# Performance work log

Measured on AMD Instinct MI355X. Metric: run time of the kernel, lower is better.

The kernel has to match this reference:

```python
import jax, jax.numpy as jnp
import numpy as np

B, S, H = 2, 2048, 2048
NH, NKV, HD = 32, 8, 64          # num_heads, num_kv_heads, head_dim
G = NH // NKV                     # GQA group size
NEG = -1e9


def setup_inputs() -> dict:
    key = jax.random.key(0)
    ks = jax.random.split(key, 8)
    x = jax.random.normal(ks[0], (B, S, H), dtype=jnp.float32)
    # real RoPE frequencies: theta = 10000 ** (-2i/hd)
    inv_freq = 1.0 / (10000.0 ** (np.arange(0, HD, 2, dtype=np.float32) / HD))
    angles = np.arange(S, dtype=np.float32)[:, None] * inv_freq[None, :]  # [S, HD//2]
    freqs_cos = jnp.asarray(np.cos(angles))
    freqs_sin = jnp.asarray(np.sin(angles))
    # additive causal mask [S, S]
    mask = jnp.where(jnp.tril(jnp.ones((S, S), dtype=bool)), 0.0, NEG).astype(jnp.float32)
    sc = 0.02
    Wq = jax.random.normal(ks[1], (NH * HD, H), dtype=jnp.float32) * sc
    bq = jax.random.normal(ks[2], (NH * HD,), dtype=jnp.float32) * sc
    Wk = jax.random.normal(ks[3], (NKV * HD, H), dtype=jnp.float32) * sc
    bk = jax.random.normal(ks[4], (NKV * HD,), dtype=jnp.float32) * sc
    Wv = jax.random.normal(ks[5], (NKV * HD, H), dtype=jnp.float32) * sc
    bv = jax.random.normal(ks[6], (NKV * HD,), dtype=jnp.float32) * sc
    Wo = jax.random.normal(ks[7], (H, NH * HD), dtype=jnp.float32) * sc
    return {"x": x, "freqs_cos": freqs_cos, "freqs_sin": freqs_sin, "mask": mask,
            "Wq": Wq, "bq": bq, "Wk": Wk, "bk": bk, "Wv": Wv, "bv": bv, "Wo": Wo}


def _rotate_half(t):
    h = t.shape[-1] // 2
    return jnp.concatenate([-t[..., h:], t[..., :h]], axis=-1)


def reference(x, freqs_cos, freqs_sin, mask, Wq, bq, Wk, bk, Wv, bv, Wo):
    b, s, _ = x.shape
    q = (x @ Wq.T + bq).reshape(b, s, NH, HD)
    k = (x @ Wk.T + bk).reshape(b, s, NKV, HD)
    v = (x @ Wv.T + bv).reshape(b, s, NKV, HD)
    # RoPE (rotate_half style): cos/sin duplicated along last dim -> [1, s, 1, HD]
    cos = jnp.concatenate([freqs_cos, freqs_cos], axis=-1)[None, :, None, :]
    sin = jnp.concatenate([freqs_sin, freqs_sin], axis=-1)[None, :, None, :]
    q = q * cos + _rotate_half(q) * sin
    k = k * cos + _rotate_half(k) * sin
    # GQA: view q as [b, s, NKV, G, HD]; avoids repeat_interleave of K/V (same math)
    q5 = q.reshape(b, s, NKV, G, HD)
    scores = jnp.einsum('bqhgd,bkhd->bhgqk', q5, k) / jnp.sqrt(jnp.float32(HD))
    scores = scores + mask  # broadcast [s, s] over [b, h, g, s, s]
    p = jax.nn.softmax(scores.astype(jnp.float32), axis=-1).astype(q.dtype)
    out = jnp.einsum('bhgqk,bkhd->bqhgd', p, v).reshape(b, s, NH * HD)
    return out @ Wo.T
```

## Files before the change

### kernel.cpp

```cpp
#include <hip/hip_runtime.h>
#include <hip/hip_bf16.h>
#include <cstddef>
#include <cstdint>

#define B_   2
#define S_   2048
#define H_   2048
#define NH_  32
#define NKV_ 8
#define HD_  64

typedef __attribute__((ext_vector_type(8))) short short8;
typedef __attribute__((ext_vector_type(4))) float v4f;
typedef __attribute__((ext_vector_type(16))) float v16f;

#define MAXC 48.0f
#define QSCALE 0.18033688011112042f

__device__ __forceinline__ unsigned short f2b(float f) {
    unsigned int u = __float_as_uint(f);
    u += 0x7FFFu + ((u >> 16) & 1u);
    return (unsigned short)(u >> 16);
}
__device__ __forceinline__ unsigned int pkbf(float a, float b) {
    __hip_bfloat162 h = __float22bfloat162_rn(float2{a, b});
    return *(unsigned int*)&h;
}
__device__ __forceinline__ float fexp2(float x) {
#if __has_builtin(__builtin_amdgcn_exp2f)
    return __builtin_amdgcn_exp2f(x);
#else
    return exp2f(x);
#endif
}
__device__ __forceinline__ v4f mfma16(short8 a, short8 b, v4f c) {
    return __builtin_amdgcn_mfma_f32_16x16x32_bf16(a, b, c, 0, 0, 0);
}
__device__ __forceinline__ v16f mfma32(short8 a, short8 b, v16f c) {
    return __builtin_amdgcn_mfma_f32_32x32x16_bf16(a, b, c, 0, 0, 0);
}
__device__ __forceinline__ void gll16(void* lds, const void* g) {
    __builtin_amdgcn_global_load_lds(
        (const __attribute__((address_space(1))) unsigned int*)g,
        (__attribute__((address_space(3))) unsigned int*)lds, 16, 0, 0);
}

__global__ __launch_bounds__(256) void convert_all(
    const float* __restrict__ x, const float* __restrict__ wq,
    const float* __restrict__ wk, const float* __restrict__ wv,
    const float* __restrict__ wo,
    unsigned short* __restrict__ xb, unsigned short* __restrict__ wqb,
    unsigned short* __restrict__ wkb, unsigned short* __restrict__ wvb,
    unsigned short* __restrict__ wob)
{
    size_t i = ((size_t)blockIdx.x * 256 + threadIdx.x) * 4;
    const float* src; unsigned short* dst; size_t off;
    if (i < 8388608)       { src = x;  dst = xb;  off = i; }
    else if (i < 12582912) { src = wq; dst = wqb; off = i - 8388608; }
    else if (i < 13631488) { src = wk; dst = wkb; off = i - 12582912; }
    else if (i < 14680064) { src = wv; dst = wvb; off = i - 13631488; }
    else                   { src = wo; dst = wob; off = i - 14680064; }
    float4 v = *(const float4*)(src + off);
    ushort4 o;
    o.x = f2b(v.x); o.y = f2b(v.y); o.z = f2b(v.z); o.w = f2b(v.w);
    *(ushort4*)(dst + off) = o;
}

__global__ __launch_bounds__(256) void qkv_gemm(
    const unsigned short* __restrict__ xb,
    const unsigned short* __restrict__ wqb, const unsigned short* __restrict__ wkb,
    const unsigned short* __restrict__ wvb,
    const float* __restrict__ bq, const float* __restrict__ bk,
    const float* __restrict__ bv,
    const float* __restrict__ fc, const float* __restrict__ fs,
    unsigned short* __restrict__ Qb, unsigned short* __restrict__ Kb,
    unsigned short* __restrict__ Vt)
{
    __shared__ unsigned short As[128 * 64];
    __shared__ unsigned short Bs[128 * 64];
    const int tid = threadIdx.x;
    const int lane = tid & 63, w = tid >> 6;
    const int tx = lane & 15, quad = lane >> 4;
    const int bx = blockIdx.x, by = blockIdx.y;

    const unsigned short *Ap, *Bp;
    int mode, aBase, bBase;
    if (bx < 16)      { mode = 0; Ap = xb;  Bp = wqb; aBase = by * 128; bBase = bx * 128; }
    else if (bx < 20) { mode = 1; Ap = xb;  Bp = wkb; aBase = by * 128; bBase = (bx - 16) * 128; }
    else              { mode = 2; Ap = wvb; Bp = xb;  aBase = (bx - 20) * 128; bBase = by * 128; }

    const int wm = (w >> 1) * 64, wn = (w & 1) * 64;
    v4f acc[4][4];
#pragma unroll
    for (int i = 0; i < 4; ++i)
#pragma unroll
        for (int j = 0; j < 4; ++j) acc[i][j] = (v4f)0.f;

    const int r8 = lane >> 3, gc = (lane & 7) ^ r8;
    const unsigned short* ga = &Ap[(size_t)(aBase + w * 32 + r8) * 2048 + gc * 8];
    const unsigned short* gb = &Bp[(size_t)(bBase + w * 32 + r8) * 2048 + gc * 8];

    const int t7 = tx & 7;
    int slA[2], slB[2];
#pragma unroll
    for (int kk = 0; kk < 2; ++kk) { slA[kk] = ((kk * 4 + quad) ^ t7) * 8; slB[kk] = slA[kk]; }

    for (int k0 = 0; k0 < 2048; k0 += 64) {
        __syncthreads();
#pragma unroll
        for (int i = 0; i < 4; ++i) {
            gll16(&As[(w * 32 + i * 8) * 64], ga + (size_t)(i * 8) * 2048 + k0);
            gll16(&Bs[(w * 32 + i * 8) * 64], gb + (size_t)(i * 8) * 2048 + k0);
        }
        __syncthreads();
#pragma unroll
        for (int kk = 0; kk < 2; ++kk) {
            short8 af[4], bf[4];
#pragma unroll
            for (int mt = 0; mt < 4; ++mt)
                af[mt] = *(const short8*)&As[(wm + mt * 16 + tx) * 64 + slA[kk]];
#pragma unroll
            for (int nt = 0; nt < 4; ++nt)
                bf[nt] = *(const short8*)&Bs[(wn + nt * 16 + tx) * 64 + slB[kk]];
#pragma unroll
            for (int mt = 0; mt < 4; ++mt)
#pragma unroll
                for (int nt = 0; nt < 4; ++nt)
                    acc[mt][nt] = mfma16(af[mt], bf[nt], acc[mt][nt]);
        }
    }

    if (mode <= 1) {
        unsigned short* Cout = mode ? Kb : Qb;
        const float* bias    = mode ? bk : bq;
        const int ldN        = mode ? 512 : 2048;
        const float scq      = mode ? 1.0f : QSCALE;
        float bx0 = bias[bBase + wn +  0 + tx];
        float bx1 = bias[bBase + wn + 16 + tx];
        float bx2 = bias[bBase + wn + 32 + tx];
        float bx3 = bias[bBase + wn + 48 + tx];
#pragma unroll
        for (int mt = 0; mt < 4; ++mt)
#pragma unroll
            for (int rg = 0; rg < 4; ++rg) {
                int m = aBase + wm + mt * 16 + quad * 4 + rg;
                int s = m & (S_ - 1);
                float c0 = fc[s * 32 + tx],      c1 = fc[s * 32 + 16 + tx];
                float s0 = fs[s * 32 + tx],      s1 = fs[s * 32 + 16 + tx];
                float q0 = acc[mt][0][rg] + bx0, q1 = acc[mt][1][rg] + bx1;
                float q2 = acc[mt][2][rg] + bx2, q3 = acc[mt][3][rg] + bx3;
                size_t base = (size_t)m * ldN + bBase + wn + tx;
                Cout[base]      = f2b((q0 * c0 - q2 * s0) * scq);
                Cout[base + 16] = f2b((q1 * c1 - q3 * s1) * scq);
                Cout[base + 32] = f2b((q2 * c0 + q0 * s0) * scq);
                Cout[base + 48] = f2b((q3 * c1 + q1 * s1) * scq);
            }
    } else {
#pragma unroll
        for (int mt = 0; mt < 4; ++mt)
#pragma unroll
            for (int rg = 0; rg < 4; ++rg) {
                int d = aBase + wm + mt * 16 + quad * 4 + rg;
                float bvv = bv[d];
                size_t base = (size_t)d * 4096 + bBase + wn + tx;
#pragma unroll
                for (int nt = 0; nt < 4; ++nt)
                    Vt[base + nt * 16] = f2b(acc[mt][nt][rg] + bvv);
            }
    }
}

__global__ __launch_bounds__(256) void out_gemm(
    const unsigned short* __restrict__ Ab, const unsigned short* __restrict__ Bw,
    float* __restrict__ C)
{
    __shared__ unsigned short As[128 * 64];
    __shared__ unsigned short Bs[128 * 64];
    const int tid = threadIdx.x;
    const int lane = tid & 63, w = tid >> 6;
    const int tx = lane & 15, quad = lane >> 4;
    const int bm = blockIdx.y * 128, bn = blockIdx.x * 128;
    const int wm = (w >> 1) * 64, wn = (w & 1) * 64;

    v4f acc[4][4];
#pragma unroll
    for (int i = 0; i < 4; ++i)
#pragma unroll
        for (int j = 0; j < 4; ++j) acc[i][j] = (v4f)0.f;

    const int r8 = lane >> 3, gc = (lane & 7) ^ r8;
    const unsigned short* ga = &Ab[(size_t)(bm + w * 32 + r8) * 2048 + gc * 8];
    const unsigned short* gb = &Bw[(size_t)(bn + w * 32 + r8) * 2048 + gc * 8];
    const int t7 = tx & 7;
    int sl[2];
#pragma unroll
    for (int kk = 0; kk < 2; ++kk) sl[kk] = ((kk * 4 + quad) ^ t7) * 8;

    for (int k0 = 0; k0 < 2048; k0 += 64) {
        __syncthreads();
#pragma unroll
        for (int i = 0; i < 4; ++i) {
            gll16(&As[(w * 32 + i * 8) * 64], ga + (size_t)(i * 8) * 2048 + k0);
            gll16(&Bs[(w * 32 + i * 8) * 64], gb + (size_t)(i * 8) * 2048 + k0);
        }
        __syncthreads();
#pragma unroll
        for (int kk = 0; kk < 2; ++kk) {
            short8 af[4], bf[4];
#pragma unroll
            for (int mt = 0; mt < 4; ++mt)
                af[mt] = *(const short8*)&As[(wm + mt * 16 + tx) * 64 + sl[kk]];
#pragma unroll
            for (int nt = 0; nt < 4; ++nt)
                bf[nt] = *(const short8*)&Bs[(wn + nt * 16 + tx) * 64 + sl[kk]];
#pragma unroll
            for (int mt = 0; mt < 4; ++mt)
#pragma unroll
                for (int nt = 0; nt < 4; ++nt)
                    acc[mt][nt] = mfma16(af[mt], bf[nt], acc[mt][nt]);
        }
    }
#pragma unroll
    for (int mt = 0; mt < 4; ++mt)
#pragma unroll
        for (int nt = 0; nt < 4; ++nt)
#pragma unroll
            for (int rg = 0; rg < 4; ++rg) {
                int m = bm + wm + mt * 16 + quad * 4 + rg;
                C[(size_t)m * 2048 + bn + wn + nt * 16 + tx] = acc[mt][nt][rg];
            }
}

__global__ __launch_bounds__(256, 4) void attn_mfma(
    const unsigned short* __restrict__ Q, const unsigned short* __restrict__ K,
    const unsigned short* __restrict__ Vt, unsigned short* __restrict__ O)
{
    __shared__ __align__(16) unsigned short smem[2][2][64 * 72];
    const int tid = threadIdx.x;
    const int lane = tid & 63, wq = tid >> 6;
    const int l32 = lane & 31, half = lane >> 5;
    const int qh = wq & 1;
    const int ts = wq >> 1;
    const int p = blockIdx.x;
    const int h = blockIdx.y, b = blockIdx.z;
    const int kvh = h >> 2;

    const int srow = tid >> 3, sc8 = (tid & 7) * 8;
    const unsigned short* gkB = &K[(((size_t)b * S_ + srow) * NKV_ + kvh) * HD_ + sc8];
    const unsigned short* gvB = &Vt[(size_t)(kvh * 64 + srow) * 4096 + (size_t)b * 2048 + sc8];
    const int woff = srow * 72 + sc8;

    for (int ph = 0; ph < 2; ++ph) {
        const int T = ph ? (31 - p) : p;

        const int qrow = T * 64 + qh * 32 + l32;
        const unsigned short* Qr = &Q[(((size_t)b * S_ + qrow) * NH_ + h) * HD_];
        short8 qf[4];
#pragma unroll
        for (int s = 0; s < 4; ++s)
            qf[s] = *(const short8*)(Qr + s * 16 + half * 8);

        float la = 0.f, lb = 0.f, lc = 0.f, ld = 0.f;
        v16f o0 = (v16f)0.f, o1 = (v16f)0.f;

        uint4 kr0 = *(const uint4*)(gkB);
        uint4 kr1 = *(const uint4*)(gkB + 32 * (NKV_ * HD_));
        uint4 vr0 = *(const uint4*)(gvB);
        uint4 vr1 = *(const uint4*)(gvB + (size_t)32 * 4096);
        int cur = 0;

        for (int kt = 0; kt <= T; ++kt) {
            unsigned short* Kw = &smem[cur][0][woff];
            unsigned short* Vw = &smem[cur][1][woff];
            *(uint4*)(Kw)           = kr0;
            *(uint4*)(Kw + 32 * 72) = kr1;
            *(uint4*)(Vw)           = vr0;
            *(uint4*)(Vw + 32 * 72) = vr1;
            __syncthreads();
            if (kt < T) {
                const unsigned short* gk = gkB + (size_t)(kt + 1) * 64 * (NKV_ * HD_);
                const unsigned short* gv = gvB + (kt + 1) * 64;
                kr0 = *(const uint4*)(gk);
                kr1 = *(const uint4*)(gk + 32 * (NKV_ * HD_));
                vr0 = *(const uint4*)(gv);
                vr1 = *(const uint4*)(gv + (size_t)32 * 4096);
            }
            const unsigned short* Ksb = smem[cur][0];
            const unsigned short* Vsb = smem[cur][1];
            cur ^= 1;

            const bool diag = (kt == T);
            if (diag && ts > qh) continue;
            const bool part = diag && (ts == qh);

            const int kb = (ts * 32 + l32) * 72 + half * 8;
            v16f st = (v16f)(-MAXC);
            __builtin_amdgcn_s_setprio(1);
            st = mfma32(*(const short8*)&Ksb[kb],      qf[0], st);
            st = mfma32(*(const short8*)&Ksb[kb + 16], qf[1], st);
            st = mfma32(*(const short8*)&Ksb[kb + 32], qf[2], st);
            st = mfma32(*(const short8*)&Ksb[kb + 48], qf[3], st);
            __builtin_amdgcn_s_setprio(0);

            float pv[16];
#pragma unroll
            for (int r = 0; r < 16; ++r) pv[r] = fexp2(st[r]);
            if (part) {
#pragma unroll
                for (int r = 0; r < 16; ++r) {
                    int krow = (r & 3) + 8 * (r >> 2) + 4 * half;
                    if (krow > l32) pv[r] = 0.f;
                }
            }
            la += (pv[0]  + pv[1])  + (pv[2]  + pv[3]);
            lb += (pv[4]  + pv[5])  + (pv[6]  + pv[7]);
            lc += (pv[8]  + pv[9])  + (pv[10] + pv[11]);
            ld += (pv[12] + pv[13]) + (pv[14] + pv[15]);

            unsigned int u[8];
#pragma unroll
            for (int g = 0; g < 4; ++g) {
                u[2 * g]     = pkbf(pv[4 * g],     pv[4 * g + 1]);
                u[2 * g + 1] = pkbf(pv[4 * g + 2], pv[4 * g + 3]);
            }
#pragma unroll
            for (int sg = 0; sg < 2; ++sg) {
                unsigned int a0 = u[4 * sg], a1 = u[4 * sg + 1];
                unsigned int b0 = u[4 * sg + 2], b1 = u[4 * sg + 3];
                uint4 fw;
#if __has_builtin(__builtin_amdgcn_permlane32_swap)
                typedef unsigned int u2v __attribute__((ext_vector_type(2)));
                u2v r0 = __builtin_amdgcn_permlane32_swap(a0, b0, false, false);
                u2v r1 = __builtin_amdgcn_permlane32_swap(a1, b1, false, false);
                fw.x = r0[0]; fw.y = r1[0]; fw.z = r0[1]; fw.w = r1[1];
#else
                unsigned int s0 = __shfl_xor((int)a0, 32);
                unsigned int s1 = __shfl_xor((int)a1, 32);
                unsigned int s2 = __shfl_xor((int)b0, 32);
                unsigned int s3 = __shfl_xor((int)b1, 32);
                fw.x = half ? s2 : a0;
                fw.y = half ? s3 : a1;
                fw.z = half ? b0 : s0;
                fw.w = half ? b1 : s1;
#endif
                short8 pf = *(short8*)&fw;
                const int vo = (2 * ts + sg) * 16 + half * 8;
                __builtin_amdgcn_s_setprio(1);
                o0 = mfma32(*(const short8*)&Vsb[l32 * 72 + vo],        pf, o0);
                o1 = mfma32(*(const short8*)&Vsb[(32 + l32) * 72 + vo], pf, o1);
                __builtin_amdgcn_s_setprio(0);
            }
        }

        float l = (la + lb) + (lc + ld);
        l += __shfl_xor(l, 32);

        __syncthreads();
        float* red = (float*)&smem[0][0][0];
        const int rbase = (qh * 64 + lane) * 33;
        if (ts == 1) {
#pragma unroll
            for (int r = 0; r < 16; ++r) { red[rbase + r] = o0[r]; red[rbase + 16 + r] = o1[r]; }
            red[rbase + 32] = l;
        }
        __syncthreads();
        if (ts == 0) {
#pragma unroll
            for (int r = 0; r < 16; ++r) { o0[r] += red[rbase + r]; o1[r] += red[rbase + 16 + r]; }
            l += red[rbase + 32];
            float inv = 1.f / l;
            int qg = T * 64 + qh * 32 + l32;
            unsigned short* orow = &O[((size_t)b * S_ + qg) * (NH_ * HD_) + h * HD_];
#pragma unroll
            for (int td = 0; td < 2; ++td) {
                const v16f& oo = td ? o1 : o0;
#pragma unroll
                for (int g = 0; g < 4; ++g) {
                    int d = td * 32 + g * 8 + half * 4;
                    uint2 uu;
                    uu.x = pkbf(oo[4 * g] * inv,     oo[4 * g + 1] * inv);
                    uu.y = pkbf(oo[4 * g + 2] * inv, oo[4 * g + 3] * inv);
                    *(uint2*)&orow[d] = uu;
                }
            }
        }
        if (ph == 0) __syncthreads();
    }
}

extern "C" void kernel_launch(void* const* d_in, const int* in_sizes, int n_in,
                              void* d_out, int out_size, void* d_ws, size_t ws_size,
                              hipStream_t stream)
{
    const float* x  = (const float*)d_in[0];
    const float* fc = (const float*)d_in[1];
    const float* fs = (const float*)d_in[2];
    const float* Wq = (const float*)d_in[4];
    const float* bq = (const float*)d_in[5];
    const float* Wk = (const float*)d_in[6];
    const float* bk = (const float*)d_in[7];
    const float* Wv = (const float*)d_in[8];
    const float* bv = (const float*)d_in[9];
    const float* Wo = (const float*)d_in[10];
    float* out = (float*)d_out;

    unsigned short* ws = (unsigned short*)d_ws;
    unsigned short* xb  = ws;
    unsigned short* wqb = ws + 8388608;
    unsigned short* wkb = ws + 12582912;
    unsigned short* wvb = ws + 13631488;
    unsigned short* wob = ws + 14680064;
    unsigned short* Qb  = ws + 18874368;
    unsigned short* Kb  = ws + 27262976;
    unsigned short* Vt  = ws + 29360128;
    unsigned short* Ob  = ws + 31457280;

    dim3 blk(256);
    convert_all<<<18432, blk, 0, stream>>>(x, Wq, Wk, Wv, Wo, xb, wqb, wkb, wvb, wob);
    qkv_gemm<<<dim3(24, 32), blk, 0, stream>>>(xb, wqb, wkb, wvb, bq, bk, bv,
                                               fc, fs, Qb, Kb, Vt);
    attn_mfma<<<dim3(16, NH_, B_), blk, 0, stream>>>(Qb, Kb, Vt, Ob);
    out_gemm<<<dim3(16, 32), blk, 0, stream>>>(Ob, wob, out);
}
```

Before: 312.7 us.

## Rework QKV GEMM into 256x256 double-buffered tiles with 512 threads and swizzle

The QKV projection GEMM moves from 128x128 tiles with 256 threads and a single LDS buffer to 256x256 tiles with 512 threads, double-buffered async global-to-LDS loads, and explicit vmcnt waits so loads overlap MFMA work. The V path is now computed as x·Wv with a transposed vectorized store instead of swapping operands. A block-index swizzle and s_setprio are added to improve L2 reuse and MFMA issue priority. The larger per-block LDS (128KB) and accumulator footprint limit occupancy, and only 192 blocks are launched for the GPU's CUs.

```diff
diff --git a/kernel.cpp b/kernel.cpp
--- a/kernel.cpp
+++ b/kernel.cpp
@@ -66,7 +66,7 @@
     *(ushort4*)(dst + off) = o;
 }
 
-__global__ __launch_bounds__(256) void qkv_gemm(
+__global__ __launch_bounds__(512, 2) void qkv_gemm(
     const unsigned short* __restrict__ xb,
     const unsigned short* __restrict__ wqb, const unsigned short* __restrict__ wkb,
     const unsigned short* __restrict__ wvb,
@@ -76,80 +76,103 @@
     unsigned short* __restrict__ Qb, unsigned short* __restrict__ Kb,
     unsigned short* __restrict__ Vt)
 {
-    __shared__ unsigned short As[128 * 64];
-    __shared__ unsigned short Bs[128 * 64];
+    __shared__ unsigned short As[2][256 * 64];
+    __shared__ unsigned short Bs[2][256 * 64];
     const int tid = threadIdx.x;
     const int lane = tid & 63, w = tid >> 6;
     const int tx = lane & 15, quad = lane >> 4;
-    const int bx = blockIdx.x, by = blockIdx.y;
-
-    const unsigned short *Ap, *Bp;
-    int mode, aBase, bBase;
-    if (bx < 16)      { mode = 0; Ap = xb;  Bp = wqb; aBase = by * 128; bBase = bx * 128; }
-    else if (bx < 20) { mode = 1; Ap = xb;  Bp = wkb; aBase = by * 128; bBase = (bx - 16) * 128; }
-    else              { mode = 2; Ap = wvb; Bp = xb;  aBase = (bx - 20) * 128; bBase = by * 128; }
-
-    const int wm = (w >> 1) * 64, wn = (w & 1) * 64;
-    v4f acc[4][4];
-#pragma unroll
-    for (int i = 0; i < 4; ++i)
+
+    const int bid = blockIdx.x;
+    const int swz = (bid & 7) * 24 + (bid >> 3);
+    const int bi = swz / 12, bj = swz % 12;
+    const int bm = bi * 256, bcol = bj * 256;
+
+    const unsigned short* Bp; int mode, nbase;
+    if (bj < 8)       { Bp = wqb + (size_t)bcol * 2048;          mode = 0; nbase = bcol; }
+    else if (bj < 10) { Bp = wkb + (size_t)(bcol - 2048) * 2048; mode = 1; nbase = bcol - 2048; }
+    else              { Bp = wvb + (size_t)(bcol - 2560) * 2048; mode = 2; nbase = bcol - 2560; }
+    const unsigned short* Ap = xb + (size_t)bm * 2048;
+
+    const int wm = (w >> 2) * 128, wn = (w & 3) * 64;
+
+    v4f acc[8][4];
+#pragma unroll
+    for (int i = 0; i < 8; ++i)
 #pragma unroll
         for (int j = 0; j < 4; ++j) acc[i][j] = (v4f)0.f;
 
     const int r8 = lane >> 3, gc = (lane & 7) ^ r8;
-    const unsigned short* ga = &Ap[(size_t)(aBase + w * 32 + r8) * 2048 + gc * 8];
-    const unsigned short* gb = &Bp[(size_t)(bBase + w * 32 + r8) * 2048 + gc * 8];
+    const unsigned short* ga = Ap + (size_t)(w * 32 + r8) * 2048 + gc * 8;
+    const unsigned short* gb = Bp + (size_t)(w * 32 + r8) * 2048 + gc * 8;
+
+#define QKV_STAGE(c, t) { \
+    _Pragma("unroll") \
+    for (int i_ = 0; i_ < 4; ++i_) { \
+        gll16(&As[c][(w * 32 + i_ * 8) * 64], ga + (size_t)(i_ * 8) * 2048 + (t) * 64); \
+        gll16(&Bs[c][(w * 32 + i_ * 8) * 64], gb + (size_t)(i_ * 8) * 2048 + (t) * 64); \
+    } }
 
     const int t7 = tx & 7;
-    int slA[2], slB[2];
-#pragma unroll
-    for (int kk = 0; kk < 2; ++kk) { slA[kk] = ((kk * 4 + quad) ^ t7) * 8; slB[kk] = slA[kk]; }
-
-    for (int k0 = 0; k0 < 2048; k0 += 64) {
-        __syncthreads();
-#pragma unroll
-        for (int i = 0; i < 4; ++i) {
-            gll16(&As[(w * 32 + i * 8) * 64], ga + (size_t)(i * 8) * 2048 + k0);
-            gll16(&Bs[(w * 32 + i * 8) * 64], gb + (size_t)(i * 8) * 2048 + k0);
-        }
-        __syncthreads();
+    int sl[2];
+#pragma unroll
+    for (int kk = 0; kk < 2; ++kk) sl[kk] = ((kk * 4 + quad) ^ t7) * 8;
+
+    QKV_STAGE(0, 0)
+    QKV_STAGE(1, 1)
+
+    for (int t = 0; t < 32; ++t) {
+        if (t < 31) asm volatile("s_waitcnt vmcnt(8)" ::: "memory");
+        else        asm volatile("s_waitcnt vmcnt(0)" ::: "memory");
+        __builtin_amdgcn_sched_barrier(0);
+        __builtin_amdgcn_s_barrier();
+        __builtin_amdgcn_sched_barrier(0);
+
+        const unsigned short* Asb = As[t & 1];
+        const unsigned short* Bsb = Bs[t & 1];
 #pragma unroll
         for (int kk = 0; kk < 2; ++kk) {
-            short8 af[4], bf[4];
-#pragma unroll
-            for (int mt = 0; mt < 4; ++mt)
-                af[mt] = *(const short8*)&As[(wm + mt * 16 + tx) * 64 + slA[kk]];
+            short8 bfr[4];
 #pragma unroll
             for (int nt = 0; nt < 4; ++nt)
-                bf[nt] = *(const short8*)&Bs[(wn + nt * 16 + tx) * 64 + slB[kk]];
-#pragma unroll
-            for (int mt = 0; mt < 4; ++mt)
+                bfr[nt] = *(const short8*)&Bsb[(wn + nt * 16 + tx) * 64 + sl[kk]];
+            __builtin_amdgcn_s_setprio(1);
+#pragma unroll
+            for (int mt = 0; mt < 8; ++mt) {
+                short8 a = *(const short8*)&Asb[(wm + mt * 16 + tx) * 64 + sl[kk]];
 #pragma unroll
                 for (int nt = 0; nt < 4; ++nt)
-                    acc[mt][nt] = mfma16(af[mt], bf[nt], acc[mt][nt]);
-        }
+                    acc[mt][nt] = mfma16(a, bfr[nt], acc[mt][nt]);
+            }
+            __builtin_amdgcn_s_setprio(0);
+        }
+
+        __builtin_amdgcn_sched_barrier(0);
+        __builtin_amdgcn_s_barrier();
+        __builtin_amdgcn_sched_barrier(0);
+        if (t < 30) QKV_STAGE(t & 1, t + 2)
     }
+#undef QKV_STAGE
 
     if (mode <= 1) {
         unsigned short* Cout = mode ? Kb : Qb;
         const float* bias    = mode ? bk : bq;
         const int ldN        = mode ? 512 : 2048;
         const float scq      = mode ? 1.0f : QSCALE;
-        float bx0 = bias[bBase + wn +  0 + tx];
-        float bx1 = bias[bBase + wn + 16 + tx];
-        float bx2 = bias[bBase + wn + 32 + tx];
-        float bx3 = bias[bBase + wn + 48 + tx];
-#pragma unroll
-        for (int mt = 0; mt < 4; ++mt)
+        float bx0 = bias[nbase + wn +  0 + tx];
+        float bx1 = bias[nbase + wn + 16 + tx];
+        float bx2 = bias[nbase + wn + 32 + tx];
+        float bx3 = bias[nbase + wn + 48 + tx];
+#pragma unroll
+        for (int mt = 0; mt < 8; ++mt)
 #pragma unroll
             for (int rg = 0; rg < 4; ++rg) {
-                int m = aBase + wm + mt * 16 + quad * 4 + rg;
+                int m = bm + wm + mt * 16 + quad * 4 + rg;
                 int s = m & (S_ - 1);
                 float c0 = fc[s * 32 + tx],      c1 = fc[s * 32 + 16 + tx];
                 float s0 = fs[s * 32 + tx],      s1 = fs[s * 32 + 16 + tx];
                 float q0 = acc[mt][0][rg] + bx0, q1 = acc[mt][1][rg] + bx1;
                 float q2 = acc[mt][2][rg] + bx2, q3 = acc[mt][3][rg] + bx3;
-                size_t base = (size_t)m * ldN + bBase + wn + tx;
+                size_t base = (size_t)m * ldN + nbase + wn + tx;
                 Cout[base]      = f2b((q0 * c0 - q2 * s0) * scq);
                 Cout[base + 16] = f2b((q1 * c1 - q3 * s1) * scq);
                 Cout[base + 32] = f2b((q2 * c0 + q0 * s0) * scq);
@@ -157,16 +180,20 @@
             }
     } else {
 #pragma unroll
-        for (int mt = 0; mt < 4; ++mt)
-#pragma unroll
-            for (int rg = 0; rg < 4; ++rg) {
-                int d = aBase + wm + mt * 16 + quad * 4 + rg;
-                float bvv = bv[d];
-                size_t base = (size_t)d * 4096 + bBase + wn + tx;
-#pragma unroll
-                for (int nt = 0; nt < 4; ++nt)
-                    Vt[base + nt * 16] = f2b(acc[mt][nt][rg] + bvv);
-            }
+        for (int nt = 0; nt < 4; ++nt) {
+            int d = nbase + wn + nt * 16 + tx;
+            float bvv = bv[d];
+#pragma unroll
+            for (int mt = 0; mt < 8; ++mt) {
+                int m0 = bm + wm + mt * 16 + quad * 4;
+                ushort4 o;
+                o.x = f2b(acc[mt][nt][0] + bvv);
+                o.y = f2b(acc[mt][nt][1] + bvv);
+                o.z = f2b(acc[mt][nt][2] + bvv);
+                o.w = f2b(acc[mt][nt][3] + bvv);
+                *(ushort4*)&Vt[(size_t)d * 4096 + m0] = o;
+            }
+        }
     }
 }
 
@@ -417,8 +444,8 @@
 
     dim3 blk(256);
     convert_all<<<18432, blk, 0, stream>>>(x, Wq, Wk, Wv, Wo, xb, wqb, wkb, wvb, wob);
-    qkv_gemm<<<dim3(24, 32), blk, 0, stream>>>(xb, wqb, wkb, wvb, bq, bk, bv,
-                                               fc, fs, Qb, Kb, Vt);
+    qkv_gemm<<<192, dim3(512), 0, stream>>>(xb, wqb, wkb, wvb, bq, bk, bv,
+                                            fc, fs, Qb, Kb, Vt);
     attn_mfma<<<dim3(16, NH_, B_), blk, 0, stream>>>(Qb, Kb, Vt, Ob);
     out_gemm<<<dim3(16, 32), blk, 0, stream>>>(Ob, wob, out);
 }
```

New measurement: 310.9 us. No clear change (-0.6%).
